# Kernel optimization log

Measured on AMD Instinct MI355X. Metric: run time of the kernel, lower is better.

The kernel has to match this reference:

```python
import jax, jax.numpy as jnp
import numpy as np
from jax.scipy.special import erf

B, S, D = 8, 512, 512
H = 8            # num_heads per half
DH = D // 2      # 256, per-branch model dim
DFF = 2048
HOUT = 2


def _layernorm(x, g, b, eps=1e-6):
    mu = jnp.mean(x, axis=-1, keepdims=True)
    var = jnp.mean(jnp.square(x - mu), axis=-1, keepdims=True)
    return (x - mu) / jnp.sqrt(var + eps) * g + b


def _rescale_dist(w):
    one = jnp.float32(1.0)
    return (one + jnp.exp(one)) / (one + jnp.exp(one - w))


def _mha(xin, wq, bq, wk, bk, wv, bv, wo, bo, maskf, adjoin, dist):
    b, s, dm = xin.shape
    dep = dm // H
    def heads(t):
        return t.reshape(b, s, H, dep).transpose(0, 2, 1, 3)  # (b,h,s,dep)
    q = heads(xin @ wq + bq)
    k = heads(xin @ wk + bk)
    v = heads(xin @ wv + bv)
    scores = jnp.einsum('bhqd,bhkd->bhqk', q, k)
    scale = jnp.sqrt(jnp.float32(dep))
    if dist is not None:
        scores = jax.nn.relu(scores) * _rescale_dist(dist) / scale
    else:
        scores = scores / scale
    scores = scores + maskf * jnp.float32(-1e9)
    if adjoin is not None:
        scores = scores + adjoin
    attn = jax.nn.softmax(scores, axis=-1)
    out = jnp.einsum('bhqk,bhkd->bhqd', attn, v).transpose(0, 2, 1, 3).reshape(b, s, dm)
    return out @ wo + bo, attn


def setup_inputs() -> dict:
    key = jax.random.key(0)
    ks = jax.random.split(key, 32)
    init = lambda k, shp: (jax.random.normal(k, shp, dtype=jnp.float32) * 0.02)
    inp = {
        'x': jax.random.normal(ks[0], (B, S, D), dtype=jnp.float32),
        'adjoin_matrix': jax.random.normal(ks[1], (B, 1, S, S), dtype=jnp.float32),
        'dist_matrix': jax.random.uniform(ks[2], (B, 1, S, S), dtype=jnp.float32),
        # mha1 (adjoin branch)
        'wq1': init(ks[3], (DH, DH)), 'bq1': jnp.zeros((DH,), jnp.float32),
        'wk1': init(ks[4], (DH, DH)), 'bk1': jnp.zeros((DH,), jnp.float32),
        'wv1': init(ks[5], (DH, DH)), 'bv1': jnp.zeros((DH,), jnp.float32),
        'wo1': init(ks[6], (DH, DH)), 'bo1': jnp.zeros((DH,), jnp.float32),
        # mha2 (distance branch)
        'wq2': init(ks[7], (DH, DH)), 'bq2': jnp.zeros((DH,), jnp.float32),
        'wk2': init(ks[8], (DH, DH)), 'bk2': jnp.zeros((DH,), jnp.float32),
        'wv2': init(ks[9], (DH, DH)), 'bv2': jnp.zeros((DH,), jnp.float32),
        'wo2': init(ks[10], (DH, DH)), 'bo2': jnp.zeros((DH,), jnp.float32),
        # BANLayer
        'vnet_w': init(ks[11], (DH, 2 * DH)), 'vnet_b': jnp.zeros((2 * DH,), jnp.float32),
        'qnet_w': init(ks[12], (DH, 2 * DH)), 'qnet_b': jnp.zeros((2 * DH,), jnp.float32),
        'h_mat': init(ks[13], (1, HOUT, 1, 2 * DH)),
        'h_bias': init(ks[14], (1, HOUT, 1, 1)),
        'bn_gamma': jnp.ones((D,), jnp.float32), 'bn_beta': jnp.zeros((D,), jnp.float32),
        'bn_mean': jnp.zeros((D,), jnp.float32), 'bn_var': jnp.ones((D,), jnp.float32),
        # LayerNorms
        'ln1_g': jnp.ones((D,), jnp.float32), 'ln1_b': jnp.zeros((D,), jnp.float32),
        'ln2_g': jnp.ones((D,), jnp.float32), 'ln2_b': jnp.zeros((D,), jnp.float32),
        # FFN
        'ffn_w1': init(ks[15], (D, DFF)), 'ffn_b1': jnp.zeros((DFF,), jnp.float32),
        'ffn_w2': init(ks[16], (DFF, D)), 'ffn_b2': jnp.zeros((D,), jnp.float32),
        # padding mask (int -> cast), 1 = masked
        'encoder_padding_mask': jax.random.randint(ks[17], (B, 1, 1, S), 0, 2, dtype=jnp.int32),
    }
    return inp


def reference(x, adjoin_matrix, dist_matrix,
              wq1, bq1, wk1, bk1, wv1, bv1, wo1, bo1,
              wq2, bq2, wk2, bk2, wv2, bv2, wo2, bo2,
              vnet_w, vnet_b, qnet_w, qnet_b, h_mat, h_bias,
              bn_gamma, bn_beta, bn_mean, bn_var,
              ln1_g, ln1_b, ln2_g, ln2_b,
              ffn_w1, ffn_b1, ffn_w2, ffn_b2,
              encoder_padding_mask):
    maskf = encoder_padding_mask.astype(jnp.float32)
    x1, x2 = jnp.split(x, 2, axis=-1)
    # local branch: adjoin bias, no distance
    x_l, aw_local = _mha(x1, wq1, bq1, wk1, bk1, wv1, bv1, wo1, bo1, maskf, adjoin_matrix, None)
    # global branch: relu + distance rescale, no adjoin
    x_g, aw_global = _mha(x2, wq2, bq2, wk2, bk2, wv2, bv2, wo2, bo2, maskf, None, dist_matrix)
    # BANLayer (h_out=2 <= c, eval mode; p_net is identity for rows=1)
    v_ = jax.nn.relu(x_l @ vnet_w + vnet_b)   # (B,S,2*DH)
    q_ = jax.nn.relu(x_g @ qnet_w + qnet_b)
    att_maps = jnp.einsum('xhyk,bvk,bqk->bhvq', h_mat, v_, q_) + h_bias  # (B,HOUT,S,S)
    logits = jnp.einsum('bvk,bhvq,bqk->bvk', v_, att_maps, q_)           # sum over h
    logits = (logits - bn_mean) / jnp.sqrt(bn_var + 1e-3) * bn_gamma + bn_beta
    attn_output = logits * jnp.concatenate([x_l, x_g], axis=-1)
    out1 = _layernorm(x + attn_output, ln1_g, ln1_b)
    h = out1 @ ffn_w1 + ffn_b1
    h = 0.5 * h * (1.0 + erf(h / jnp.sqrt(jnp.float32(2.0))))  # exact gelu
    ffn_out = h @ ffn_w2 + ffn_b2
    out2 = _layernorm(out1 + ffn_out, ln2_g, ln2_b)
    return (out2, aw_local, aw_global)
```

## Files before the change

kernel.cpp:

```cpp
#include <hip/hip_runtime.h>
#include <hip/hip_bf16.h>

typedef __hip_bfloat16 bf16;
typedef __attribute__((ext_vector_type(8))) short bf16x8;
typedef __attribute__((ext_vector_type(4))) float f32x4;

#define BB 8
#define SS 512
#define DD 512
#define NH 8
#define DHm 256
#define DFF 2048

__device__ __forceinline__ void gl_lds16(const void* g, void* l) {
  __builtin_amdgcn_global_load_lds((const __attribute__((address_space(1))) void*)g,
                                   (__attribute__((address_space(3))) void*)l, 16, 0, 0);
}

__device__ __forceinline__ bf16x8 cvt8(const float* p) {
  union { bf16x8 v; bf16 h[8]; } u;
  float4 f0 = *(const float4*)p, f1 = *(const float4*)(p + 4);
  u.h[0]=__float2bfloat16(f0.x); u.h[1]=__float2bfloat16(f0.y);
  u.h[2]=__float2bfloat16(f0.z); u.h[3]=__float2bfloat16(f0.w);
  u.h[4]=__float2bfloat16(f1.x); u.h[5]=__float2bfloat16(f1.y);
  u.h[6]=__float2bfloat16(f1.z); u.h[7]=__float2bfloat16(f1.w);
  return u.v;
}

template<int BM, int BN, int SMODE, int BIASM, int ACT>
__global__ __launch_bounds__(256)
void gemm2(const bf16* __restrict__ A, const bf16* __restrict__ B,
           const float* __restrict__ bias, float* __restrict__ Cf,
           bf16* __restrict__ Cb, int K, int lda, int ldb, int ldc,
           long long sA, long long sB, long long sC, int sBias)
{
  __shared__ bf16 As[BM * 32];
  __shared__ bf16 Bs[BN * 32];
  const int t = threadIdx.x, lane = t & 63, wave = t >> 6;
  const int l15 = lane & 15, quad = lane >> 4;
  constexpr int WMT = BM / 32, WNT = BN / 32;
  const int wm = (wave & 1) * (BM / 2), wn = (wave >> 1) * (BN / 2);
  const int row0 = blockIdx.y * BM, col0 = blockIdx.x * BN;
  const bf16* Ab = A + (long long)blockIdx.z * sA + (long long)row0 * lda;
  const bf16* Bb = B + (long long)blockIdx.z * sB + (long long)col0 * ldb;
  const int srow = wave * 16 + (lane >> 2), skc = (lane & 3) << 3;

  f32x4 acc[WMT][WNT] = {};

  for (int k0 = 0; k0 < K; k0 += 32) {
#pragma unroll
    for (int j = 0; j < BM / 64; j++)
      gl_lds16(Ab + (long long)(srow + j * 64) * lda + k0 + skc,
               (char*)As + wave * 1024 + j * 4096);
#pragma unroll
    for (int j = 0; j < BN / 64; j++)
      gl_lds16(Bb + (long long)(srow + j * 64) * ldb + k0 + skc,
               (char*)Bs + wave * 1024 + j * 4096);
    __syncthreads();
    bf16x8 af[WMT], bfr[WNT];
#pragma unroll
    for (int i = 0; i < WMT; i++) af[i]  = *(const bf16x8*)&As[(wm + i * 16 + l15) * 32 + quad * 8];
#pragma unroll
    for (int j = 0; j < WNT; j++) bfr[j] = *(const bf16x8*)&Bs[(wn + j * 16 + l15) * 32 + quad * 8];
#pragma unroll
    for (int i = 0; i < WMT; i++)
#pragma unroll
      for (int j = 0; j < WNT; j++)
        acc[i][j] = __builtin_amdgcn_mfma_f32_16x16x32_bf16(af[i], bfr[j], acc[i][j], 0, 0, 0);
    __syncthreads();
  }

  float sb = 0.f;
  if (BIASM == 2) sb = bias[0] + bias[1];
#pragma unroll
  for (int i = 0; i < WMT; i++)
#pragma unroll
    for (int j = 0; j < WNT; j++) {
      int col = col0 + wn + j * 16 + l15;
      float bv = (BIASM == 1) ? bias[(long long)blockIdx.z * sBias + col] : sb;
#pragma unroll
      for (int r = 0; r < 4; r++) {
        int row = row0 + wm + i * 16 + (quad << 2) + r;
        float v = acc[i][j][r] + bv;
        if (ACT == 1) v = fmaxf(v, 0.f);
        if (ACT == 2) v = 0.5f * v * (1.f + erff(v * 0.70710678118654752f));
        long long ci = (long long)blockIdx.z * sC + (long long)row * ldc + col;
        if (SMODE & 1) Cf[ci] = v;
        if (SMODE & 2) Cb[ci] = __float2bfloat16(v);
      }
    }
}

__global__ __launch_bounds__(256, 3)
void attn_fused(const bf16* __restrict__ QKV1, const bf16* __restrict__ QKV2,
                const int* __restrict__ mask,
                const float* __restrict__ adjoin, const float* __restrict__ dist,
                float* __restrict__ awl, float* __restrict__ awg,
                bf16* __restrict__ ctx1, bf16* __restrict__ ctx2)
{
  const int qt = blockIdx.x, h = blockIdx.y, zz = blockIdx.z;
  const int b = zz & 7, branch = zz >> 3;
  const bf16* __restrict__ QKV = branch ? QKV2 : QKV1;
  const float* __restrict__ extra = branch ? dist : adjoin;
  float* __restrict__ aw = branch ? awg : awl;
  bf16* __restrict__ ctx = branch ? ctx2 : ctx1;

  const int t = threadIdx.x, lane = t & 63, wave = t >> 6;
  const int l15 = lane & 15, quad = lane >> 4;
  __shared__ bf16x8 Vt[64][32];
  alignas(16) __shared__ bf16 Pl[4][2048];

  {
    const bf16* Vb = QKV + (long long)b * SS * 768 + 512 + h * 32;
    int dep = t & 31;
#pragma unroll
    for (int j8 = 0; j8 < 8; j8++) {
      int blk = (t >> 5) + (j8 << 3);
      union { bf16x8 v; bf16 hh[8]; } u;
#pragma unroll
      for (int i = 0; i < 8; i++)
        u.hh[i] = Vb[(long long)(blk * 8 + i) * 768 + dep];
      Vt[blk][dep] = u.v;
    }
  }

  const int q0 = qt * 64 + wave * 16;
  const bf16* Qb = QKV + ((long long)(b * SS + q0)) * 768 + h * 32;
  bf16x8 qfrag = *(const bf16x8*)(Qb + (long long)l15 * 768 + quad * 8);
  __syncthreads();

  const float scale_inv = 0.17677669529663688f;
  const bf16* Kb = QKV + (long long)b * SS * 768 + 256 + h * 32;
  const float* Eb = extra + ((long long)b * SS + q0) * SS;

  float rsum[4] = {0.f, 0.f, 0.f, 0.f};
#pragma unroll
  for (int kc = 0; kc < 32; kc++) {
    const int kpos = kc * 16 + l15;
    bf16x8 kfrag = *(const bf16x8*)(Kb + (long long)kpos * 768 + quad * 8);
    f32x4 a = __builtin_amdgcn_mfma_f32_16x16x32_bf16(qfrag, kfrag, f32x4{0.f,0.f,0.f,0.f}, 0, 0, 0);
    float mval = (float)mask[b * SS + kpos] * -1e9f;
#pragma unroll
    for (int r = 0; r < 4; r++) {
      float s = a[r];
      float ev = Eb[(long long)(quad * 4 + r) * SS + kpos];
      if (branch == 0) {
        s = s * scale_inv + mval + ev;
      } else {
        float resc = 3.7182818284590452f / (1.f + __expf(1.f - ev));
        s = fmaxf(s, 0.f) * resc * scale_inv + mval;
      }
      rsum[r] += __expf(s);
    }
  }
  float rsi[4];
#pragma unroll
  for (int r = 0; r < 4; r++) {
    float v = rsum[r];
    v += __shfl_xor(v, 1, 16);
    v += __shfl_xor(v, 2, 16);
    v += __shfl_xor(v, 4, 16);
    v += __shfl_xor(v, 8, 16);
    rsi[r] = 1.f / v;
  }

  f32x4 oacc[2] = {};
  bf16* Pw = Pl[wave];
  const int rkey = ((l15 >> 2) ^ l15) & 3;
  float* awp = aw + (((long long)(b * NH + h) * SS + q0)) * SS;

#pragma unroll
  for (int c = 0; c < 4; c++) {
#pragma unroll
    for (int kcl = 0; kcl < 8; kcl++) {
      const int kc = c * 8 + kcl;
      const int kpos = kc * 16 + l15;
      bf16x8 kfrag = *(const bf16x8*)(Kb + (long long)kpos * 768 + quad * 8);
      f32x4 a = __builtin_amdgcn_mfma_f32_16x16x32_bf16(qfrag, kfrag, f32x4{0.f,0.f,0.f,0.f}, 0, 0, 0);
      float mval = (float)mask[b * SS + kpos] * -1e9f;
#pragma unroll
      for (int r = 0; r < 4; r++) {
        float s = a[r];
        float ev = Eb[(long long)(quad * 4 + r) * SS + kpos];
        if (branch == 0) {
          s = s * scale_inv + mval + ev;
        } else {
          float resc = 3.7182818284590452f / (1.f + __expf(1.f - ev));
          s = fmaxf(s, 0.f) * resc * scale_inv + mval;
        }
        float p = __expf(s) * rsi[r];
        __builtin_nontemporal_store(p, awp + (long long)(quad * 4 + r) * SS + kpos);
        const int key = (quad ^ r) & 3;
        const int off = (quad * 4 + r) * 256 + (((kcl * 16 + l15) * 2) ^ (key << 5));
        *(bf16*)((char*)Pw + off) = __float2bfloat16(p);
      }
    }
    __builtin_amdgcn_s_setprio(1);
#pragma unroll
    for (int k2 = 0; k2 < 4; k2++) {
      const int off = l15 * 256 + ((k2 * 64 + quad * 16) ^ (rkey << 5));
      bf16x8 afr = *(const bf16x8*)((const char*)Pw + off);
      const int blk = (c * 4 + k2) * 4 + quad;
      oacc[0] = __builtin_amdgcn_mfma_f32_16x16x32_bf16(afr, Vt[blk][l15],      oacc[0], 0, 0, 0);
      oacc[1] = __builtin_amdgcn_mfma_f32_16x16x32_bf16(afr, Vt[blk][16 + l15], oacc[1], 0, 0, 0);
    }
    __builtin_amdgcn_s_setprio(0);
  }

#pragma unroll
  for (int n = 0; n < 2; n++)
#pragma unroll
    for (int r = 0; r < 4; r++) {
      int q = q0 + quad * 4 + r;
      ctx[(long long)(b * SS + q) * DHm + h * 32 + n * 16 + l15] =
          __float2bfloat16(oacc[n][r]);
    }
}

__device__ __forceinline__ void tr_tile(const float* __restrict__ src, bf16* __restrict__ dst,
                                        int K, int N, int tile) {
  __shared__ float tl[32][33];
  int tilesN = N >> 5;
  int tk = tile / tilesN, tn = tile % tilesN;
  int c = threadIdx.x & 31, r0 = threadIdx.x >> 5;
#pragma unroll
  for (int i = 0; i < 4; i++) {
    int r = r0 + i * 8;
    tl[r][c] = src[(long long)(tk * 32 + r) * N + tn * 32 + c];
  }
  __syncthreads();
#pragma unroll
  for (int i = 0; i < 4; i++) {
    int r = r0 + i * 8;
    dst[(long long)(tn * 32 + r) * K + tk * 32 + c] = __float2bfloat16(tl[c][r]);
  }
}

__global__ __launch_bounds__(256)
void pack_all(const float* wq1, const float* wk1, const float* wv1,
              const float* wq2, const float* wk2, const float* wv2,
              const float* wo1, const float* wo2,
              const float* vnet_w, const float* qnet_w,
              const float* ffn_w1, const float* ffn_w2,
              const float* bq1, const float* bk1, const float* bv1,
              const float* bq2, const float* bk2, const float* bv2,
              const float* bo1, const float* bo2,
              const float* vnet_b, const float* qnet_b,
              const float* x,
              bf16* WB1, bf16* WB2, bf16* woT1, bf16* woT2,
              bf16* vnetT, bf16* qnetT, bf16* f1T, bf16* f2T,
              float* BB1v, float* BB2v, float* BOv, float* VQb, bf16* xb)
{
  int blk = blockIdx.x;
  if (blk < 64)        { tr_tile(wq1, WB1,            256, 256, blk); return; }
  if (blk < 128)       { tr_tile(wk1, WB1 + 256*256,  256, 256, blk-64); return; }
  if (blk < 192)       { tr_tile(wv1, WB1 + 512*256,  256, 256, blk-128); return; }
  if (blk < 256)       { tr_tile(wq2, WB2,            256, 256, blk-192); return; }
  if (blk < 320)       { tr_tile(wk2, WB2 + 256*256,  256, 256, blk-256); return; }
  if (blk < 384)       { tr_tile(wv2, WB2 + 512*256,  256, 256, blk-320); return; }
  if (blk < 448)       { tr_tile(wo1, woT1,           256, 256, blk-384); return; }
  if (blk < 512)       { tr_tile(wo2, woT2,           256, 256, blk-448); return; }
  if (blk < 640)       { tr_tile(vnet_w, vnetT,       256, 512, blk-512); return; }
  if (blk < 768)       { tr_tile(qnet_w, qnetT,       256, 512, blk-640); return; }
  if (blk < 1792)      { tr_tile(ffn_w1, f1T,         512, 2048, blk-768); return; }
  if (blk < 2816)      { tr_tile(ffn_w2, f2T,         2048, 512, blk-1792); return; }
  if (blk < 3840) {
    long long i0 = (long long)(blk - 2816) * 2048 + threadIdx.x * 8;
    *(bf16x8*)(xb + i0) = cvt8(x + i0);
    return;
  }
  if (blk < 3846) {
    int b = blk - 3840;
    const float* src = b==0?bq1 : b==1?bk1 : b==2?bv1 : b==3?bq2 : b==4?bk2 : bv2;
    float* dst = (b < 3 ? BB1v : BB2v) + (b % 3) * 256;
    dst[threadIdx.x] = src[threadIdx.x];
    return;
  }
  if (blk < 3848) {
    int b = blk - 3846;
    BOv[b * 256 + threadIdx.x] = (b ? bo2 : bo1)[threadIdx.x];
    return;
  }
  {
    int b = blk - 3848;
    const float* src = (b < 2) ? vnet_b : qnet_b;
    VQb[b * 256 + threadIdx.x] = src[(b & 1) * 256 + threadIdx.x];
  }
}

__global__ __launch_bounds__(256)
void tr_qn(const bf16* __restrict__ Qn, bf16* __restrict__ QnT)
{
  int b = blockIdx.z, tk = blockIdx.y, tn = blockIdx.x;
  __shared__ bf16 tl[32][33];
  int c = threadIdx.x & 31, r0 = threadIdx.x >> 5;
  const bf16* src = Qn + (long long)b * 512 * 512;
  bf16* dst = QnT + (long long)b * 512 * 512;
#pragma unroll
  for (int i = 0; i < 4; i++) { int r = r0 + i * 8; tl[r][c] = src[(tk * 32 + r) * 512 + tn * 32 + c]; }
  __syncthreads();
#pragma unroll
  for (int i = 0; i < 4; i++) { int r = r0 + i * 8; dst[(tn * 32 + r) * 512 + tk * 32 + c] = tl[c][r]; }
}

__global__ __launch_bounds__(256)
void vh_kernel(const bf16* __restrict__ v_, const float* __restrict__ hmat,
               bf16* __restrict__ vh, int n)
{
  int i = blockIdx.x * 256 + threadIdx.x;
  if (i < n) {
    int c = i & (DD - 1);
    vh[i] = __float2bfloat16(__bfloat162float(v_[i]) * (hmat[c] + hmat[DD + c]));
  }
}

__global__ __launch_bounds__(256)
void bn_gate_ln1_kernel(const float* __restrict__ x, const bf16* __restrict__ vbuf,
                        const float* __restrict__ T, const float* __restrict__ xl,
                        const float* __restrict__ xg,
                        const float* __restrict__ bng, const float* __restrict__ bnb,
                        const float* __restrict__ bnm, const float* __restrict__ bnv,
                        const float* __restrict__ lng, const float* __restrict__ lnb,
                        float* __restrict__ out1, bf16* __restrict__ out1b)
{
  const int row = blockIdx.x;
  const int t = threadIdx.x;
  const int lane = t & 63, wave = t >> 6;
  __shared__ float red[8];
  float val[2];
#pragma unroll
  for (int i = 0; i < 2; i++) {
    int c = t + i * 256;
    long long idx = (long long)row * DD + c;
    float lg = __bfloat162float(vbuf[idx]) * T[idx];
    float bn = (lg - bnm[c]) / sqrtf(bnv[c] + 1e-3f) * bng[c] + bnb[c];
    float gate = (c < DHm) ? xl[(long long)row * DHm + c] : xg[(long long)row * DHm + (c - DHm)];
    val[i] = x[idx] + bn * gate;
  }
  float s = val[0] + val[1];
#pragma unroll
  for (int o = 32; o > 0; o >>= 1) s += __shfl_xor(s, o);
  if (lane == 0) red[wave] = s;
  __syncthreads();
  float mu = (red[0] + red[1] + red[2] + red[3]) * (1.f / 512.f);
  float d0 = val[0] - mu, d1 = val[1] - mu;
  float vs = d0 * d0 + d1 * d1;
#pragma unroll
  for (int o = 32; o > 0; o >>= 1) vs += __shfl_xor(vs, o);
  if (lane == 0) red[4 + wave] = vs;
  __syncthreads();
  float inv = 1.f / sqrtf((red[4] + red[5] + red[6] + red[7]) * (1.f / 512.f) + 1e-6f);
  float o0 = d0 * inv * lng[t] + lnb[t];
  float o1 = d1 * inv * lng[t + 256] + lnb[t + 256];
  out1[(long long)row * DD + t] = o0;
  out1[(long long)row * DD + t + 256] = o1;
  out1b[(long long)row * DD + t] = __float2bfloat16(o0);
  out1b[(long long)row * DD + t + 256] = __float2bfloat16(o1);
}

__global__ __launch_bounds__(256)
void ln2_kernel(const float* __restrict__ a, const float* __restrict__ b2,
                const float* __restrict__ g, const float* __restrict__ bta,
                float* __restrict__ out)
{
  const int row = blockIdx.x;
  const int t = threadIdx.x;
  const int lane = t & 63, wave = t >> 6;
  __shared__ float red[8];
  float v0 = a[(long long)row * DD + t]       + b2[(long long)row * DD + t];
  float v1 = a[(long long)row * DD + t + 256] + b2[(long long)row * DD + t + 256];
  float s = v0 + v1;
#pragma unroll
  for (int o = 32; o > 0; o >>= 1) s += __shfl_xor(s, o);
  if (lane == 0) red[wave] = s;
  __syncthreads();
  float mu = (red[0] + red[1] + red[2] + red[3]) * (1.f / 512.f);
  float d0 = v0 - mu, d1 = v1 - mu;
  float vs = d0 * d0 + d1 * d1;
#pragma unroll
  for (int o = 32; o > 0; o >>= 1) vs += __shfl_xor(vs, o);
  if (lane == 0) red[4 + wave] = vs;
  __syncthreads();
  float inv = 1.f / sqrtf((red[4] + red[5] + red[6] + red[7]) * (1.f / 512.f) + 1e-6f);
  out[(long long)row * DD + t]       = d0 * inv * g[t]       + bta[t];
  out[(long long)row * DD + t + 256] = d1 * inv * g[t + 256] + bta[t + 256];
}

extern "C" void kernel_launch(void* const* d_in, const int* in_sizes, int n_in,
                              void* d_out, int out_size, void* d_ws, size_t ws_size,
                              hipStream_t stream) {
  const float* x      = (const float*)d_in[0];
  const float* adjoin = (const float*)d_in[1];
  const float* dist   = (const float*)d_in[2];
  const float* wq1=(const float*)d_in[3],  *bq1=(const float*)d_in[4];
  const float* wk1=(const float*)d_in[5],  *bk1=(const float*)d_in[6];
  const float* wv1=(const float*)d_in[7],  *bv1=(const float*)d_in[8];
  const float* wo1=(const float*)d_in[9],  *bo1=(const float*)d_in[10];
  const float* wq2=(const float*)d_in[11], *bq2=(const float*)d_in[12];
  const float* wk2=(const float*)d_in[13], *bk2=(const float*)d_in[14];
  const float* wv2=(const float*)d_in[15], *bv2=(const float*)d_in[16];
  const float* wo2=(const float*)d_in[17], *bo2=(const float*)d_in[18];
  const float* vnet_w=(const float*)d_in[19], *vnet_b=(const float*)d_in[20];
  const float* qnet_w=(const float*)d_in[21], *qnet_b=(const float*)d_in[22];
  const float* h_mat=(const float*)d_in[23], *h_bias=(const float*)d_in[24];
  const float* bn_g=(const float*)d_in[25], *bn_b=(const float*)d_in[26];
  const float* bn_m=(const float*)d_in[27], *bn_v=(const float*)d_in[28];
  const float* ln1_g=(const float*)d_in[29], *ln1_b=(const float*)d_in[30];
  const float* ln2_g=(const float*)d_in[31], *ln2_b=(const float*)d_in[32];
  const float* ffn_w1=(const float*)d_in[33], *ffn_b1=(const float*)d_in[34];
  const float* ffn_w2=(const float*)d_in[35], *ffn_b2=(const float*)d_in[36];
  const int* mask = (const int*)d_in[37];

  char* base = (char*)d_ws;
  size_t off = 0;
  auto alloc = [&](size_t bytes) { char* p = base + off; off += (bytes + 255) & ~(size_t)255; return p; };
  bf16*  xb    = (bf16*) alloc(4096LL*512*2);
  bf16*  WB1   = (bf16*) alloc(768*256*2);
  bf16*  WB2   = (bf16*) alloc(768*256*2);
  float* BB1v  = (float*)alloc(768*4);
  float* BB2v  = (float*)alloc(768*4);
  float* BOv   = (float*)alloc(512*4);
  float* VQb   = (float*)alloc(1024*4);
  bf16*  woT1  = (bf16*) alloc(256*256*2);
  bf16*  woT2  = (bf16*) alloc(256*256*2);
  bf16*  vnetT = (bf16*) alloc(512*256*2);
  bf16*  qnetT = (bf16*) alloc(512*256*2);
  bf16*  f1T   = (bf16*) alloc(2048*512*2);
  bf16*  f2T   = (bf16*) alloc(512*2048*2);
  bf16*  QKV1  = (bf16*) alloc(4096LL*768*2);
  bf16*  QKV2  = (bf16*) alloc(4096LL*768*2);
  bf16*  CTX   = (bf16*) alloc(4096LL*256*2);
  bf16*  CTX2  = (bf16*) alloc(4096LL*256*2);
  float* XL    = (float*)alloc(4096LL*256*4);
  float* XG    = (float*)alloc(4096LL*256*4);
  bf16*  XLb   = (bf16*) alloc(4096LL*256*2);
  bf16*  XGb   = (bf16*) alloc(4096LL*256*2);
  bf16*  Vn    = (bf16*) alloc(4096LL*512*2);
  bf16*  Qn    = (bf16*) alloc(4096LL*512*2);
  bf16*  QnT   = (bf16*) alloc(4096LL*512*2);
  bf16*  VH    = (bf16*) alloc(4096LL*512*2);
  bf16*  G     = (bf16*) alloc(8LL*512*512*2);
  float* T     = (float*)alloc(4096LL*512*4);
  float* OUT1  = (float*)alloc(4096LL*512*4);
  bf16*  OUT1b = (bf16*) alloc(4096LL*512*2);
  bf16*  H     = (bf16*) alloc(4096LL*2048*2);
  float* FFNO  = (float*)alloc(4096LL*512*4);

  float* out2 = (float*)d_out;
  float* awl  = out2 + 2097152LL;
  float* awg  = awl + 16777216LL;

  const int MR = BB * SS;
  const long long GST = (long long)SS * SS;

  pack_all<<<dim3(3852), 256, 0, stream>>>(
      wq1, wk1, wv1, wq2, wk2, wv2, wo1, wo2, vnet_w, qnet_w, ffn_w1, ffn_w2,
      bq1, bk1, bv1, bq2, bk2, bv2, bo1, bo2, vnet_b, qnet_b, x,
      WB1, WB2, woT1, woT2, vnetT, qnetT, f1T, f2T, BB1v, BB2v, BOv, VQb, xb);

  gemm2<128,128,2,1,0><<<dim3(6, 32, 2), 256, 0, stream>>>(
      xb, WB1, BB1v, nullptr, QKV1, 256, 512, 256, 768,
      256LL, 768LL*256, 4096LL*768, 768);

  attn_fused<<<dim3(8, NH, 16), 256, 0, stream>>>(
      QKV1, QKV2, mask, adjoin, dist, awl, awg, CTX, CTX2);

  gemm2<64,64,3,1,0><<<dim3(4, 64, 2), 256, 0, stream>>>(
      CTX, woT1, BOv, XL, XLb, 256, 256, 256, 256,
      4096LL*256, 256LL*256, 4096LL*256, 256);

  gemm2<64,64,2,1,1><<<dim3(8, 64, 2), 256, 0, stream>>>(
      XLb, vnetT, VQb, nullptr, Vn, 256, 256, 256, 512,
      4096LL*256, 512LL*256, 4096LL*512, 512);

  vh_kernel<<<dim3((MR * DD) / 256), 256, 0, stream>>>(Vn, h_mat, VH, MR * DD);
  tr_qn<<<dim3(16, 16, BB), 256, 0, stream>>>(Qn, QnT);
  gemm2<64,64,2,2,0><<<dim3(8, 8, BB), 256, 0, stream>>>(
      VH, Qn, h_bias, nullptr, G, 512, 512, 512, 512, GST, GST, GST, 0);
  gemm2<64,64,1,0,0><<<dim3(8, 8, BB), 256, 0, stream>>>(
      G, QnT, nullptr, T, nullptr, 512, 512, 512, 512, GST, GST, GST, 0);

  bn_gate_ln1_kernel<<<dim3(MR), 256, 0, stream>>>(
      x, Vn, T, XL, XG, bn_g, bn_b, bn_m, bn_v, ln1_g, ln1_b, OUT1, OUT1b);

  gemm2<128,128,2,1,2><<<dim3(16, 32, 1), 256, 0, stream>>>(
      OUT1b, f1T, ffn_b1, nullptr, H, 512, 512, 512, 2048, 0, 0, 0, 0);
  gemm2<64,128,1,1,0><<<dim3(4, 64, 1), 256, 0, stream>>>(
      H, f2T, ffn_b2, FFNO, nullptr, 2048, 2048, 2048, 512, 0, 0, 0, 0);

  ln2_kernel<<<dim3(MR), 256, 0, stream>>>(OUT1, FFNO, ln2_g, ln2_b, out2);
}
```

Before: 522.4 us.

## Precompute attention bias fragments and write V pre-transposed from QKV GEMM

Adds an eprep kernel that converts adjoin/dist matrices (with mask and distance rescale folded in) into a per-fragment f32x4 layout so attention reads them coalesced. The QKV GEMM epilogue writes V in the transposed tile layout attention needs, which is loaded via global_load_lds, and the h_mat scaling is fused into the vnet GEMM epilogue, removing vh_kernel. The cost is an extra 32 MB intermediate buffer that is written once and read twice, doubling bias traffic in exchange for coalescing and less ALU work.

```diff
diff --git a/kernel.cpp b/kernel.cpp
--- a/kernel.cpp
+++ b/kernel.cpp
@@ -27,12 +27,13 @@
   return u.v;
 }
 
-template<int BM, int BN, int SMODE, int BIASM, int ACT>
+template<int BM, int BN, int SMODE, int BIASM, int ACT, int VTM>
 __global__ __launch_bounds__(256)
 void gemm2(const bf16* __restrict__ A, const bf16* __restrict__ B,
            const float* __restrict__ bias, float* __restrict__ Cf,
            bf16* __restrict__ Cb, int K, int lda, int ldb, int ldc,
-           long long sA, long long sB, long long sC, int sBias)
+           long long sA, long long sB, long long sC, int sBias,
+           bf16* __restrict__ Cb2, const float* __restrict__ cscale)
 {
   __shared__ bf16 As[BM * 32];
   __shared__ bf16 Bs[BN * 32];
@@ -78,30 +79,86 @@
     for (int j = 0; j < WNT; j++) {
       int col = col0 + wn + j * 16 + l15;
       float bv = (BIASM == 1) ? bias[(long long)blockIdx.z * sBias + col] : sb;
+      float vv[4];
 #pragma unroll
       for (int r = 0; r < 4; r++) {
-        int row = row0 + wm + i * 16 + (quad << 2) + r;
         float v = acc[i][j][r] + bv;
         if (ACT == 1) v = fmaxf(v, 0.f);
         if (ACT == 2) v = 0.5f * v * (1.f + erff(v * 0.70710678118654752f));
-        long long ci = (long long)blockIdx.z * sC + (long long)row * ldc + col;
-        if (SMODE & 1) Cf[ci] = v;
-        if (SMODE & 2) Cb[ci] = __float2bfloat16(v);
+        vv[r] = v;
+      }
+      const int rowb = row0 + wm + i * 16 + (quad << 2);
+      if (VTM == 1 && col >= 512) {
+        int hh = (col - 512) >> 5, dep = (col - 512) & 31;
+        int bidx = rowb >> 9, kpos = rowb & 511;
+        long long vo = ((((long long)blockIdx.z * 8 + bidx) * 8 + hh) * 64 + (kpos >> 3)) * 32 + dep;
+        bf16 h0 = __float2bfloat16(vv[0]), h1 = __float2bfloat16(vv[1]);
+        bf16 h2 = __float2bfloat16(vv[2]), h3 = __float2bfloat16(vv[3]);
+        short4 pk;
+        pk.x = *(short*)&h0; pk.y = *(short*)&h1; pk.z = *(short*)&h2; pk.w = *(short*)&h3;
+        *(short4*)(Cb2 + vo * 8 + (kpos & 7)) = pk;
+      } else {
+#pragma unroll
+        for (int r = 0; r < 4; r++) {
+          long long ci = (long long)blockIdx.z * sC + (long long)(rowb + r) * ldc + col;
+          if (SMODE & 1) Cf[ci] = vv[r];
+          if (SMODE & 2) Cb[ci] = __float2bfloat16(vv[r]);
+          if (VTM == 2) Cb2[ci] = __float2bfloat16(vv[r] * cscale[col]);
+        }
       }
     }
 }
 
+__global__ __launch_bounds__(256)
+void eprep(const float* __restrict__ adjoin, const float* __restrict__ dist,
+           const int* __restrict__ mask, float* __restrict__ EP)
+{
+  const int qt = blockIdx.x, kt = blockIdx.y, zz = blockIdx.z;
+  const int b = zz & 7, branch = zz >> 3;
+  const float* E = (branch ? dist : adjoin) + ((long long)b * SS + qt * 64) * SS + kt * 128;
+  __shared__ float tile[64][129];
+  const int t = threadIdx.x;
+  const int r0 = t >> 2, c0 = (t & 3) * 32;
+#pragma unroll
+  for (int jj = 0; jj < 8; jj++) {
+    float4 f = *(const float4*)(E + (long long)r0 * SS + c0 + jj * 4);
+    tile[r0][c0 + jj * 4 + 0] = f.x; tile[r0][c0 + jj * 4 + 1] = f.y;
+    tile[r0][c0 + jj * 4 + 2] = f.z; tile[r0][c0 + jj * 4 + 3] = f.w;
+  }
+  __syncthreads();
+  const int lane = t & 63, wq = t >> 6, l15 = lane & 15, quad = lane >> 4;
+  const float scale_inv = 0.17677669529663688f;
+  f32x4* out = (f32x4*)EP;
+#pragma unroll
+  for (int kcl = 0; kcl < 8; kcl++) {
+    int kk = kcl * 16 + l15;
+    f32x4 o;
+    if (branch == 0) {
+      float mv = (float)mask[b * SS + kt * 128 + kk] * -1e9f;
+#pragma unroll
+      for (int r = 0; r < 4; r++)
+        o[r] = tile[wq * 16 + quad * 4 + r][kk] + mv;
+    } else {
+#pragma unroll
+      for (int r = 0; r < 4; r++) {
+        float ev = tile[wq * 16 + quad * 4 + r][kk];
+        o[r] = 3.7182818284590452f / (1.f + __expf(1.f - ev)) * scale_inv;
+      }
+    }
+    out[((((long long)zz * 8 + qt) * 4 + wq) * 32 + (kt * 8 + kcl)) * 64 + lane] = o;
+  }
+}
+
 __global__ __launch_bounds__(256, 3)
 void attn_fused(const bf16* __restrict__ QKV1, const bf16* __restrict__ QKV2,
-                const int* __restrict__ mask,
-                const float* __restrict__ adjoin, const float* __restrict__ dist,
+                const bf16* __restrict__ VT, const int* __restrict__ mask,
+                const float* __restrict__ EP,
                 float* __restrict__ awl, float* __restrict__ awg,
                 bf16* __restrict__ ctx1, bf16* __restrict__ ctx2)
 {
   const int qt = blockIdx.x, h = blockIdx.y, zz = blockIdx.z;
   const int b = zz & 7, branch = zz >> 3;
   const bf16* __restrict__ QKV = branch ? QKV2 : QKV1;
-  const float* __restrict__ extra = branch ? dist : adjoin;
   float* __restrict__ aw = branch ? awg : awl;
   bf16* __restrict__ ctx = branch ? ctx2 : ctx1;
 
@@ -109,20 +166,16 @@
   const int l15 = lane & 15, quad = lane >> 4;
   __shared__ bf16x8 Vt[64][32];
   alignas(16) __shared__ bf16 Pl[4][2048];
-
-  {
-    const bf16* Vb = QKV + (long long)b * SS * 768 + 512 + h * 32;
-    int dep = t & 31;
-#pragma unroll
-    for (int j8 = 0; j8 < 8; j8++) {
-      int blk = (t >> 5) + (j8 << 3);
-      union { bf16x8 v; bf16 hh[8]; } u;
-#pragma unroll
-      for (int i = 0; i < 8; i++)
-        u.hh[i] = Vb[(long long)(blk * 8 + i) * 768 + dep];
-      Vt[blk][dep] = u.v;
-    }
-  }
+  __shared__ float mvalf[512];
+
+  const bf16* VTs = VT + ((long long)zz * 8 + h) * 16384;
+#pragma unroll
+  for (int j = 0; j < 8; j++)
+    gl_lds16(VTs + (long long)t * 8 + j * 2048, (char*)Vt + wave * 1024 + j * 4096);
+
+  { int2 m2 = *(const int2*)(mask + b * SS + t * 2);
+    mvalf[t * 2]     = (float)m2.x * -1e9f;
+    mvalf[t * 2 + 1] = (float)m2.y * -1e9f; }
 
   const int q0 = qt * 64 + wave * 16;
   const bf16* Qb = QKV + ((long long)(b * SS + q0)) * 768 + h * 32;
@@ -131,25 +184,20 @@
 
   const float scale_inv = 0.17677669529663688f;
   const bf16* Kb = QKV + (long long)b * SS * 768 + 256 + h * 32;
-  const float* Eb = extra + ((long long)b * SS + q0) * SS;
+  const f32x4* Ep = (const f32x4*)EP + (((long long)zz * 8 + qt) * 4 + wave) * 2048;
 
   float rsum[4] = {0.f, 0.f, 0.f, 0.f};
 #pragma unroll
   for (int kc = 0; kc < 32; kc++) {
     const int kpos = kc * 16 + l15;
     bf16x8 kfrag = *(const bf16x8*)(Kb + (long long)kpos * 768 + quad * 8);
+    f32x4 e4 = Ep[kc * 64 + lane];
     f32x4 a = __builtin_amdgcn_mfma_f32_16x16x32_bf16(qfrag, kfrag, f32x4{0.f,0.f,0.f,0.f}, 0, 0, 0);
-    float mval = (float)mask[b * SS + kpos] * -1e9f;
+    float mv = (branch == 0) ? 0.f : mvalf[kpos];
 #pragma unroll
     for (int r = 0; r < 4; r++) {
-      float s = a[r];
-      float ev = Eb[(long long)(quad * 4 + r) * SS + kpos];
-      if (branch == 0) {
-        s = s * scale_inv + mval + ev;
-      } else {
-        float resc = 3.7182818284590452f / (1.f + __expf(1.f - ev));
-        s = fmaxf(s, 0.f) * resc * scale_inv + mval;
-      }
+      float s = (branch == 0) ? fmaf(a[r], scale_inv, e4[r])
+                              : fmaf(fmaxf(a[r], 0.f), e4[r], mv);
       rsum[r] += __expf(s);
     }
   }
@@ -176,18 +224,13 @@
       const int kc = c * 8 + kcl;
       const int kpos = kc * 16 + l15;
       bf16x8 kfrag = *(const bf16x8*)(Kb + (long long)kpos * 768 + quad * 8);
+      f32x4 e4 = Ep[kc * 64 + lane];
       f32x4 a = __builtin_amdgcn_mfma_f32_16x16x32_bf16(qfrag, kfrag, f32x4{0.f,0.f,0.f,0.f}, 0, 0, 0);
-      float mval = (float)mask[b * SS + kpos] * -1e9f;
+      float mv = (branch == 0) ? 0.f : mvalf[kpos];
 #pragma unroll
       for (int r = 0; r < 4; r++) {
-        float s = a[r];
-        float ev = Eb[(long long)(quad * 4 + r) * SS + kpos];
-        if (branch == 0) {
-          s = s * scale_inv + mval + ev;
-        } else {
-          float resc = 3.7182818284590452f / (1.f + __expf(1.f - ev));
-          s = fmaxf(s, 0.f) * resc * scale_inv + mval;
-        }
+        float s = (branch == 0) ? fmaf(a[r], scale_inv, e4[r])
+                                : fmaf(fmaxf(a[r], 0.f), e4[r], mv);
         float p = __expf(s) * rsi[r];
         __builtin_nontemporal_store(p, awp + (long long)(quad * 4 + r) * SS + kpos);
         const int key = (quad ^ r) & 3;
@@ -246,10 +289,11 @@
               const float* bq2, const float* bk2, const float* bv2,
               const float* bo1, const float* bo2,
               const float* vnet_b, const float* qnet_b,
+              const float* h_mat,
               const float* x,
               bf16* WB1, bf16* WB2, bf16* woT1, bf16* woT2,
               bf16* vnetT, bf16* qnetT, bf16* f1T, bf16* f2T,
-              float* BB1v, float* BB2v, float* BOv, float* VQb, bf16* xb)
+              float* BB1v, float* BB2v, float* BOv, float* VQb, float* HSv, bf16* xb)
 {
   int blk = blockIdx.x;
   if (blk < 64)        { tr_tile(wq1, WB1,            256, 256, blk); return; }
@@ -281,10 +325,16 @@
     BOv[b * 256 + threadIdx.x] = (b ? bo2 : bo1)[threadIdx.x];
     return;
   }
-  {
+  if (blk < 3852) {
     int b = blk - 3848;
     const float* src = (b < 2) ? vnet_b : qnet_b;
     VQb[b * 256 + threadIdx.x] = src[(b & 1) * 256 + threadIdx.x];
+    return;
+  }
+  {
+    int t = threadIdx.x;
+    HSv[t]       = h_mat[t]       + h_mat[512 + t];
+    HSv[t + 256] = h_mat[256 + t] + h_mat[768 + t];
   }
 }
 
@@ -301,17 +351,6 @@
   __syncthreads();
 #pragma unroll
   for (int i = 0; i < 4; i++) { int r = r0 + i * 8; dst[(tn * 32 + r) * 512 + tk * 32 + c] = tl[c][r]; }
-}
-
-__global__ __launch_bounds__(256)
-void vh_kernel(const bf16* __restrict__ v_, const float* __restrict__ hmat,
-               bf16* __restrict__ vh, int n)
-{
-  int i = blockIdx.x * 256 + threadIdx.x;
-  if (i < n) {
-    int c = i & (DD - 1);
-    vh[i] = __float2bfloat16(__bfloat162float(v_[i]) * (hmat[c] + hmat[DD + c]));
-  }
 }
 
 __global__ __launch_bounds__(256)
@@ -421,6 +460,7 @@
   float* BB2v  = (float*)alloc(768*4);
   float* BOv   = (float*)alloc(512*4);
   float* VQb   = (float*)alloc(1024*4);
+  float* HSv   = (float*)alloc(512*4);
   bf16*  woT1  = (bf16*) alloc(256*256*2);
   bf16*  woT2  = (bf16*) alloc(256*256*2);
   bf16*  vnetT = (bf16*) alloc(512*256*2);
@@ -429,6 +469,8 @@
   bf16*  f2T   = (bf16*) alloc(512*2048*2);
   bf16*  QKV1  = (bf16*) alloc(4096LL*768*2);
   bf16*  QKV2  = (bf16*) alloc(4096LL*768*2);
+  bf16*  VTb   = (bf16*) alloc(2LL*8*8*512*32*2);
+  float* EP    = (float*)alloc(33554432);
   bf16*  CTX   = (bf16*) alloc(4096LL*256*2);
   bf16*  CTX2  = (bf16*) alloc(4096LL*256*2);
   float* XL    = (float*)alloc(4096LL*256*4);
@@ -453,40 +495,41 @@
   const int MR = BB * SS;
   const long long GST = (long long)SS * SS;
 
-  pack_all<<<dim3(3852), 256, 0, stream>>>(
+  pack_all<<<dim3(3853), 256, 0, stream>>>(
       wq1, wk1, wv1, wq2, wk2, wv2, wo1, wo2, vnet_w, qnet_w, ffn_w1, ffn_w2,
-      bq1, bk1, bv1, bq2, bk2, bv2, bo1, bo2, vnet_b, qnet_b, x,
-      WB1, WB2, woT1, woT2, vnetT, qnetT, f1T, f2T, BB1v, BB2v, BOv, VQb, xb);
-
-  gemm2<128,128,2,1,0><<<dim3(6, 32, 2), 256, 0, stream>>>(
+      bq1, bk1, bv1, bq2, bk2, bv2, bo1, bo2, vnet_b, qnet_b, h_mat, x,
+      WB1, WB2, woT1, woT2, vnetT, qnetT, f1T, f2T, BB1v, BB2v, BOv, VQb, HSv, xb);
+
+  eprep<<<dim3(8, 4, 16), 256, 0, stream>>>(adjoin, dist, mask, EP);
+
+  gemm2<128,128,2,1,0,1><<<dim3(6, 32, 2), 256, 0, stream>>>(
       xb, WB1, BB1v, nullptr, QKV1, 256, 512, 256, 768,
-      256LL, 768LL*256, 4096LL*768, 768);
+      256LL, 768LL*256, 4096LL*768, 768, VTb, nullptr);
 
   attn_fused<<<dim3(8, NH, 16), 256, 0, stream>>>(
-      QKV1, QKV2, mask, adjoin, dist, awl, awg, CTX, CTX2);
-
-  gemm2<64,64,3,1,0><<<dim3(4, 64, 2), 256, 0, stream>>>(
+      QKV1, QKV2, VTb, mask, EP, awl, awg, CTX, CTX2);
+
+  gemm2<64,64,3,1,0,0><<<dim3(4, 64, 2), 256, 0, stream>>>(
       CTX, woT1, BOv, XL, XLb, 256, 256, 256, 256,
-      4096LL*256, 256LL*256, 4096LL*256, 256);
-
-  gemm2<64,64,2,1,1><<<dim3(8, 64, 2), 256, 0, stream>>>(
+      4096LL*256, 256LL*256, 4096LL*256, 256, nullptr, nullptr);
+
+  gemm2<64,64,2,1,1,2><<<dim3(8, 64, 2), 256, 0, stream>>>(
       XLb, vnetT, VQb, nullptr, Vn, 256, 256, 256, 512,
-      4096LL*256, 512LL*256, 4096LL*512, 512);
-
-  vh_kernel<<<dim3((MR * DD) / 256), 256, 0, stream>>>(Vn, h_mat, VH, MR * DD);
+      4096LL*256, 512LL*256, 4096LL*512, 512, VH, HSv);
+
   tr_qn<<<dim3(16, 16, BB), 256, 0, stream>>>(Qn, QnT);
-  gemm2<64,64,2,2,0><<<dim3(8, 8, BB), 256, 0, stream>>>(
-      VH, Qn, h_bias, nullptr, G, 512, 512, 512, 512, GST, GST, GST, 0);
-  gemm2<64,64,1,0,0><<<dim3(8, 8, BB), 256, 0, stream>>>(
-      G, QnT, nullptr, T, nullptr, 512, 512, 512, 512, GST, GST, GST, 0);
+  gemm2<64,64,2,2,0,0><<<dim3(8, 8, BB), 256, 0, stream>>>(
+      VH, Qn, h_bias, nullptr, G, 512, 512, 512, 512, GST, GST, GST, 0, nullptr, nullptr);
+  gemm2<64,64,1,0,0,0><<<dim3(8, 8, BB), 256, 0, stream>>>(
+      G, QnT, nullptr, T, nullptr, 512, 512, 512, 512, GST, GST, GST, 0, nullptr, nullptr);
 
   bn_gate_ln1_kernel<<<dim3(MR), 256, 0, stream>>>(
       x, Vn, T, XL, XG, bn_g, bn_b, bn_m, bn_v, ln1_g, ln1_b, OUT1, OUT1b);
 
-  gemm2<128,128,2,1,2><<<dim3(16, 32, 1), 256, 0, stream>>>(
-      OUT1b, f1T, ffn_b1, nullptr, H, 512, 512, 512, 2048, 0, 0, 0, 0);
-  gemm2<64,128,1,1,0><<<dim3(4, 64, 1), 256, 0, stream>>>(
-      H, f2T, ffn_b2, FFNO, nullptr, 2048, 2048, 2048, 512, 0, 0, 0, 0);
+  gemm2<128,128,2,1,2,0><<<dim3(16, 32, 1), 256, 0, stream>>>(
+      OUT1b, f1T, ffn_b1, nullptr, H, 512, 512, 512, 2048, 0, 0, 0, 0, nullptr, nullptr);
+  gemm2<64,128,1,1,0,0><<<dim3(4, 64, 1), 256, 0, stream>>>(
+      H, f2T, ffn_b2, FFNO, nullptr, 2048, 2048, 2048, 512, 0, 0, 0, 0, nullptr, nullptr);
 
   ln2_kernel<<<dim3(MR), 256, 0, stream>>>(OUT1, FFNO, ln2_g, ln2_b, out2);
 }
```

Result: faster. 490.7 us (-6.1%).
